# Performance work log

Measured on AMD Instinct MI355X. Metric: run time of the kernel, lower is better.

Reference implementation:

```python
import jax, jax.numpy as jnp
import numpy as np

# Model dims (match init_kwargs / input_specs)
L, D, H, F = 4, 1024, 16, 4096   # layers, d_model, heads, ffn hidden
B, S = 4, 1024                    # batch, seq_len
HD = D // H                       # head dim = 64
K = 8                             # context-mask band width (k=8, 2//k == 0)
LN_EPS = 1e-5


def setup_inputs():
    key = jax.random.key(0)
    ks = jax.random.split(key, 16)
    s = 0.02  # init scale for weights
    return {
        "src":   jax.random.normal(ks[0], (B, S, D), jnp.float32),
        # stacked per-layer params (leading dim L)
        "Wqkv":  jax.random.normal(ks[1], (L, 3 * D, D), jnp.float32) * s,
        "bqkv":  jnp.zeros((L, 3 * D), jnp.float32),
        "Wo":    jax.random.normal(ks[2], (L, D, D), jnp.float32) * s,
        "bo":    jnp.zeros((L, D), jnp.float32),
        "W1":    jax.random.normal(ks[3], (L, F, D), jnp.float32) * s,
        "b1":    jnp.zeros((L, F), jnp.float32),
        "W2":    jax.random.normal(ks[4], (L, D, F), jnp.float32) * s,
        "b2":    jnp.zeros((L, D), jnp.float32),
        "ln1_w": jnp.ones((L, D), jnp.float32),
        "ln1_b": jnp.zeros((L, D), jnp.float32),
        "ln2_w": jnp.ones((L, D), jnp.float32),
        "ln2_b": jnp.zeros((L, D), jnp.float32),
    }


def _layer_norm(x, g, b):
    m = jnp.mean(x, axis=-1, keepdims=True)
    v = jnp.mean(jnp.square(x - m), axis=-1, keepdims=True)
    return (x - m) * jax.lax.rsqrt(v + LN_EPS) * g + b


def _context_mask(sz):
    # row i allows keys j with i <= j < i + K (clamped into range); 0 allowed, -inf masked
    i = jnp.arange(sz)[:, None]
    j = jnp.arange(sz)[None, :]
    return jnp.where((j >= i) & (j < i + K), 0.0, -jnp.inf).astype(jnp.float32)


def reference(src, Wqkv, bqkv, Wo, bo, W1, b1, W2, b2, ln1_w, ln1_b, ln2_w, ln2_b):
    mask = _context_mask(S)  # [S, S] additive mask
    scale = 1.0 / jnp.sqrt(jnp.float32(HD))
    x = src  # [B, S, D] (batch-first; equivalent to torch's permute round-trip)
    for l in range(L):
        # --- self-attention (post-norm, dropout=0) ---
        qkv = jnp.einsum('bsd,ed->bse', x, Wqkv[l]) + bqkv[l]  # [B,S,3D]
        q, k, v = jnp.split(qkv, 3, axis=-1)
        q = q.reshape(B, S, H, HD).transpose(0, 2, 1, 3)  # [B,H,S,HD]
        k = k.reshape(B, S, H, HD).transpose(0, 2, 1, 3)
        v = v.reshape(B, S, H, HD).transpose(0, 2, 1, 3)
        scores = jnp.einsum('bhqd,bhkd->bhqk', q, k) * scale + mask
        attn = jax.nn.softmax(scores, axis=-1)
        o = jnp.einsum('bhqk,bhkd->bhqd', attn, v)
        o = o.transpose(0, 2, 1, 3).reshape(B, S, D)
        o = jnp.einsum('bsd,ed->bse', o, Wo[l]) + bo[l]
        x = _layer_norm(x + o, ln1_w[l], ln1_b[l])
        # --- feed-forward, exact (erf) gelu ---
        h = jax.nn.gelu(jnp.einsum('bsd,fd->bsf', x, W1[l]) + b1[l], approximate=False)
        h = jnp.einsum('bsf,df->bsd', h, W2[l]) + b2[l]
        x = _layer_norm(x + h, ln2_w[l], ln2_b[l])
    return x
```

## Files before the change

kernel.cpp:

```cpp
#include <hip/hip_runtime.h>

#define LNUM 4
#define DMODEL 1024
#define NHEAD 16
#define FDIM 4096
#define BATCH 4
#define SEQ 1024
#define HDIM 64
#define KBAND 8
#define MROWS (BATCH * SEQ)

typedef __attribute__((ext_vector_type(8))) __bf16 bf16x8;
typedef __attribute__((ext_vector_type(4))) float f32x4;

__device__ __forceinline__ unsigned short f2bf(float f) {
  unsigned int u = __builtin_bit_cast(unsigned int, f);
  u = u + 0x7fffu + ((u >> 16) & 1u);
  return (unsigned short)(u >> 16);
}
__device__ __forceinline__ float bf2f(unsigned short h) {
  unsigned int u = ((unsigned int)h) << 16;
  return __builtin_bit_cast(float, u);
}

#define GLOAD16(gp, lp)                                                        \
  __builtin_amdgcn_global_load_lds(                                            \
      (const __attribute__((address_space(1))) void*)(gp),                     \
      (__attribute__((address_space(3))) void*)(lp), 16, 0, 0)

__global__ __launch_bounds__(256) void cvt_bf16(const float* __restrict__ in,
                                                unsigned short* __restrict__ out,
                                                long n) {
  long i = ((long)blockIdx.x * 256 + threadIdx.x) * 4;
  if (i + 3 < n) {
    float4 v = *reinterpret_cast<const float4*>(in + i);
    ushort4 o;
    o.x = f2bf(v.x);
    o.y = f2bf(v.y);
    o.z = f2bf(v.z);
    o.w = f2bf(v.w);
    *reinterpret_cast<ushort4*>(out + i) = o;
  }
}

#define BAR_MID()                                                              \
  __builtin_amdgcn_s_barrier();                                                \
  asm volatile("s_waitcnt lgkmcnt(0)" ::: "memory");                           \
  __builtin_amdgcn_sched_barrier(0)

#define BAR_END()                                                              \
  __builtin_amdgcn_s_barrier();                                                \
  __builtin_amdgcn_sched_barrier(0)

template <int EPI>
__global__ __launch_bounds__(512, 2) void gemm256(const unsigned short* __restrict__ A,
                                                  const unsigned short* __restrict__ W,
                                                  const float* __restrict__ bias,
                                                  unsigned short* __restrict__ Cout,
                                                  int Ndim, int Kdim, int Ks) {
  __shared__ unsigned short As[2][16384];
  __shared__ unsigned short Bs[2][16384];
  const int tid = threadIdx.x;
  const int wave = tid >> 6;
  const int lane = tid & 63;
  const int wm = wave >> 2;
  const int wn = wave & 3;

  const int gx = gridDim.x, gy = gridDim.y;
  const int nwg = gx * gy;
  const int lin = blockIdx.x + blockIdx.y * gx;
  const int q8 = nwg >> 3, r8 = nwg & 7;
  const int xcd = lin & 7, cidx = lin >> 3;
  const int cbase = (xcd < r8) ? xcd * (q8 + 1) : r8 * (q8 + 1) + (xcd - r8) * q8;
  const int swz = cbase + cidx;
  const int bm0 = (swz % gy) * 256;
  const int bn0 = (swz / gy) * 256;
  const int kz0 = blockIdx.z * Ks;

  const int r0 = tid >> 3;
  const int c0 = (((tid & 7) ^ ((tid >> 3) & 7)) << 3);
  const size_t rowstep = (size_t)64 * Kdim;

#define STAGEH(MAT, rowg, buf, LDSARR, h, kt)                                  \
  do {                                                                         \
    const unsigned short* g = MAT + (size_t)((rowg) + (h) * 128 + r0) * Kdim + \
                              kz0 + (kt) * 64 + c0;                            \
    char* lb = (char*)&LDSARR[buf][0] + (h) * 16384 + wave * 1024;             \
    GLOAD16(g, lb);                                                            \
    GLOAD16(g + rowstep, lb + 8192);                                           \
  } while (0)

  const int fr = lane & 15;
  const int kc = (lane >> 4) * 8;
  const int fsw = (fr & 7) << 3;
  bf16x8 A0[2][4], A1[2][4], Bv[2][2];
  f32x4 acc[2][2][4][2] = {};

#define RD_A(SET, buf, rh)                                                     \
  _Pragma("unroll") for (int ks = 0; ks < 2; ++ks)                             \
      _Pragma("unroll") for (int fi = 0; fi < 4; ++fi)                         \
      SET[ks][fi] = *reinterpret_cast<const bf16x8*>(                          \
          &As[buf][(wm * 128 + (rh) * 64 + fi * 16 + fr) * 64 +                \
                   ((ks * 32 + kc) ^ fsw)]);

#define RD_B(buf, ch)                                                          \
  _Pragma("unroll") for (int ks = 0; ks < 2; ++ks)                             \
      _Pragma("unroll") for (int fj = 0; fj < 2; ++fj)                         \
      Bv[ks][fj] = *reinterpret_cast<const bf16x8*>(                           \
          &Bs[buf][(wn * 64 + (ch) * 32 + fj * 16 + fr) * 64 +                 \
                   ((ks * 32 + kc) ^ fsw)]);

#define MFMA_Q(rh, ch, ASET)                                                   \
  __builtin_amdgcn_s_setprio(1);                                               \
  _Pragma("unroll") for (int ks = 0; ks < 2; ++ks)                             \
      _Pragma("unroll") for (int fi = 0; fi < 4; ++fi)                         \
      _Pragma("unroll") for (int fj = 0; fj < 2; ++fj)                         \
      acc[rh][ch][fi][fj] = __builtin_amdgcn_mfma_f32_16x16x32_bf16(           \
          ASET[ks][fi], Bv[ks][fj], acc[rh][ch][fi][fj], 0, 0, 0);             \
  __builtin_amdgcn_s_setprio(0)

  const int nt = Ks >> 6;
  STAGEH(A, bm0, 0, As, 0, 0);
  STAGEH(A, bm0, 0, As, 1, 0);
  STAGEH(W, bn0, 0, Bs, 0, 0);
  STAGEH(W, bn0, 0, Bs, 1, 0);
  STAGEH(A, bm0, 1, As, 0, 1);
  STAGEH(A, bm0, 1, As, 1, 1);
  STAGEH(W, bn0, 1, Bs, 0, 1);
  asm volatile("s_waitcnt vmcnt(6)" ::: "memory");
  BAR_END();

  const int npair = nt >> 1;
  for (int i = 0; i < npair; ++i) {
    const int t1 = 2 * i + 1, t2 = 2 * i + 2, t3 = 2 * i + 3;
    const bool pf = (t2 < nt);
    RD_A(A0, 0, 0);
    RD_B(0, 0);
    STAGEH(W, bn0, 1, Bs, 1, t1);
    BAR_MID();
    MFMA_Q(0, 0, A0);
    BAR_END();

    RD_A(A1, 0, 1);
    BAR_MID();
    MFMA_Q(1, 0, A1);
    BAR_END();

    RD_B(0, 1);
    if (pf) STAGEH(A, bm0, 0, As, 0, t2);
    BAR_MID();
    MFMA_Q(1, 1, A1);
    BAR_END();

    if (pf) {
      STAGEH(A, bm0, 0, As, 1, t2);
      STAGEH(W, bn0, 0, Bs, 0, t2);
    }
    BAR_MID();
    MFMA_Q(0, 1, A0);
    if (pf)
      asm volatile("s_waitcnt vmcnt(6)" ::: "memory");
    else
      asm volatile("s_waitcnt vmcnt(0)" ::: "memory");
    BAR_END();

    RD_A(A0, 1, 0);
    RD_B(1, 0);
    if (pf) STAGEH(W, bn0, 0, Bs, 1, t2);
    BAR_MID();
    MFMA_Q(0, 0, A0);
    BAR_END();

    RD_A(A1, 1, 1);
    BAR_MID();
    MFMA_Q(1, 0, A1);
    BAR_END();

    RD_B(1, 1);
    if (pf) STAGEH(A, bm0, 1, As, 0, t3);
    BAR_MID();
    MFMA_Q(1, 1, A1);
    BAR_END();

    if (pf) {
      STAGEH(A, bm0, 1, As, 1, t3);
      STAGEH(W, bn0, 1, Bs, 0, t3);
    }
    BAR_MID();
    MFMA_Q(0, 1, A0);
    if (pf) asm volatile("s_waitcnt vmcnt(6)" ::: "memory");
    BAR_END();
  }

#undef STAGEH
#undef RD_A
#undef RD_B
#undef MFMA_Q

  const int rr = (lane >> 4) * 4;
  const int cc = lane & 15;
  const bool addb = (EPI != 2) || (blockIdx.z == 0);
  unsigned short* outZ =
      Cout + (EPI == 2 ? (size_t)blockIdx.z * ((size_t)gy * 256) * Ndim : 0);
#pragma unroll
  for (int rh = 0; rh < 2; ++rh)
#pragma unroll
    for (int ch = 0; ch < 2; ++ch)
#pragma unroll
      for (int fj = 0; fj < 2; ++fj) {
        const int n = bn0 + wn * 64 + ch * 32 + fj * 16 + cc;
        const float bv = addb ? bias[n] : 0.0f;
#pragma unroll
        for (int fi = 0; fi < 4; ++fi)
#pragma unroll
          for (int r = 0; r < 4; ++r) {
            const int m = bm0 + wm * 128 + rh * 64 + fi * 16 + rr + r;
            float v = acc[rh][ch][fi][fj][r] + bv;
            if (EPI == 1) v = 0.5f * v * (1.0f + erff(v * 0.70710678118654752f));
            outZ[(size_t)m * Ndim + n] = f2bf(v);
          }
      }
}

__global__ __launch_bounds__(256) void attn_band(const unsigned short* __restrict__ qkv,
                                                 unsigned short* __restrict__ outp) {
  const int gw = blockIdx.x * 4 + (threadIdx.x >> 6);
  const int lane = threadIdx.x & 63;
  const int q = gw & (SEQ - 1);
  const int bh = gw >> 10;
  const int h = bh & (NHEAD - 1);
  const int b = bh >> 4;
  const size_t row0 = (size_t)(b * SEQ + q);
  const size_t stride = 3 * DMODEL;
  const float qv = bf2f(qkv[row0 * stride + h * HDIM + lane]);

  float sc[KBAND];
  float mx = -1e30f;
#pragma unroll
  for (int jj = 0; jj < KBAND; ++jj) {
    const int j = q + jj;
    const int jc = (j < SEQ) ? j : (SEQ - 1);
    float kv = bf2f(qkv[(size_t)(b * SEQ + jc) * stride + DMODEL + h * HDIM + lane]);
    float p = qv * kv;
#pragma unroll
    for (int m = 32; m; m >>= 1) p += __shfl_xor(p, m);
    p *= 0.125f;
    p = (j < SEQ) ? p : -1e30f;
    sc[jj] = p;
    mx = fmaxf(mx, p);
  }
  float denom = 0.f;
  float ov = 0.f;
#pragma unroll
  for (int jj = 0; jj < KBAND; ++jj) {
    const int j = q + jj;
    const int jc = (j < SEQ) ? j : (SEQ - 1);
    float p = __expf(sc[jj] - mx);
    p = (j < SEQ) ? p : 0.f;
    denom += p;
    ov += p * bf2f(qkv[(size_t)(b * SEQ + jc) * stride + 2 * DMODEL + h * HDIM + lane]);
  }
  ov /= denom;
  outp[row0 * DMODEL + h * HDIM + lane] = f2bf(ov);
}

__global__ __launch_bounds__(256) void add_ln4(const float* __restrict__ resid,
                                               const unsigned short* __restrict__ part,
                                               const float* __restrict__ gw,
                                               const float* __restrict__ gb,
                                               float* __restrict__ xf,
                                               unsigned short* __restrict__ xb) {
  const int row = blockIdx.x;
  const int tid = threadIdx.x;
  const size_t slab = (size_t)MROWS * DMODEL;
  const float* rp = resid + (size_t)row * DMODEL;
  const unsigned short* pp = part + (size_t)row * DMODEL;
  float v[4];
  float s = 0.f, s2 = 0.f;
#pragma unroll
  for (int i = 0; i < 4; ++i) {
    const int idx = tid + i * 256;
    float a = rp[idx];
#pragma unroll
    for (int z = 0; z < 4; ++z) a += bf2f(pp[z * slab + idx]);
    v[i] = a;
    s += a;
    s2 += a * a;
  }
#pragma unroll
  for (int m = 32; m; m >>= 1) {
    s += __shfl_xor(s, m);
    s2 += __shfl_xor(s2, m);
  }
  __shared__ float wsm[8];
  const int wave = tid >> 6, lane = tid & 63;
  if (lane == 0) {
    wsm[wave] = s;
    wsm[4 + wave] = s2;
  }
  __syncthreads();
  s = wsm[0] + wsm[1] + wsm[2] + wsm[3];
  s2 = wsm[4] + wsm[5] + wsm[6] + wsm[7];
  const float mean = s * (1.f / DMODEL);
  const float var = s2 * (1.f / DMODEL) - mean * mean;
  const float rstd = rsqrtf(var + 1e-5f);
#pragma unroll
  for (int i = 0; i < 4; ++i) {
    const int idx = tid + i * 256;
    const float y = (v[i] - mean) * rstd * gw[idx] + gb[idx];
    xf[(size_t)row * DMODEL + idx] = y;
    xb[(size_t)row * DMODEL + idx] = f2bf(y);
  }
}

extern "C" void kernel_launch(void* const* d_in, const int* in_sizes, int n_in,
                              void* d_out, int out_size, void* d_ws, size_t ws_size,
                              hipStream_t stream) {
  const float* src  = (const float*)d_in[0];
  const float* Wqkv = (const float*)d_in[1];
  const float* bqkv = (const float*)d_in[2];
  const float* Wo   = (const float*)d_in[3];
  const float* bo   = (const float*)d_in[4];
  const float* W1   = (const float*)d_in[5];
  const float* b1   = (const float*)d_in[6];
  const float* W2   = (const float*)d_in[7];
  const float* b2   = (const float*)d_in[8];
  const float* ln1w = (const float*)d_in[9];
  const float* ln1b = (const float*)d_in[10];
  const float* ln2w = (const float*)d_in[11];
  const float* ln2b = (const float*)d_in[12];
  float* out = (float*)d_out;

  char* p = (char*)d_ws;
  unsigned short* wqkv_b = (unsigned short*)p; p += (size_t)LNUM * 3072 * 1024 * 2;
  unsigned short* wo_b   = (unsigned short*)p; p += (size_t)LNUM * 1024 * 1024 * 2;
  unsigned short* w1_b   = (unsigned short*)p; p += (size_t)LNUM * 4096 * 1024 * 2;
  unsigned short* w2_b   = (unsigned short*)p; p += (size_t)LNUM * 1024 * 4096 * 2;
  float*          xf     = (float*)p;          p += (size_t)MROWS * DMODEL * 4;
  unsigned short* xb     = (unsigned short*)p; p += (size_t)MROWS * DMODEL * 2;
  char* R = p;
  unsigned short* qkvb = (unsigned short*)R;
  unsigned short* aob  = (unsigned short*)(R + (size_t)MROWS * 3 * DMODEL * 2);
  unsigned short* hb   = (unsigned short*)R;
  unsigned short* part = (unsigned short*)(R + (size_t)MROWS * 4096 * 2);
  p = R + (size_t)MROWS * 4096 * 2 + (size_t)4 * MROWS * DMODEL * 2;
  if (ws_size < (size_t)(p - (char*)d_ws)) return;

  cvt_bf16<<<(long)LNUM * 3072 * 1024 / 1024, 256, 0, stream>>>(Wqkv, wqkv_b, (long)LNUM * 3072 * 1024);
  cvt_bf16<<<(long)LNUM * 1024 * 1024 / 1024, 256, 0, stream>>>(Wo, wo_b, (long)LNUM * 1024 * 1024);
  cvt_bf16<<<(long)LNUM * 4096 * 1024 / 1024, 256, 0, stream>>>(W1, w1_b, (long)LNUM * 4096 * 1024);
  cvt_bf16<<<(long)LNUM * 1024 * 4096 / 1024, 256, 0, stream>>>(W2, w2_b, (long)LNUM * 1024 * 4096);
  cvt_bf16<<<(long)MROWS * DMODEL / 1024, 256, 0, stream>>>(src, xb, (long)MROWS * DMODEL);

  for (int l = 0; l < LNUM; ++l) {
    gemm256<0><<<dim3(3072 / 256, MROWS / 256, 1), 512, 0, stream>>>(
        xb, wqkv_b + (size_t)l * 3072 * 1024, bqkv + l * 3072, qkvb, 3072, 1024, 1024);
    attn_band<<<(BATCH * NHEAD * SEQ) / 4, 256, 0, stream>>>(qkvb, aob);
    gemm256<2><<<dim3(1024 / 256, MROWS / 256, 4), 512, 0, stream>>>(
        aob, wo_b + (size_t)l * 1024 * 1024, bo + l * 1024, part, 1024, 1024, 256);
    add_ln4<<<MROWS, 256, 0, stream>>>(l == 0 ? src : xf, part,
                                       ln1w + l * DMODEL, ln1b + l * DMODEL, xf, xb);
    gemm256<1><<<dim3(FDIM / 256, MROWS / 256, 1), 512, 0, stream>>>(
        xb, w1_b + (size_t)l * 4096 * 1024, b1 + l * FDIM, hb, FDIM, 1024, 1024);
    gemm256<2><<<dim3(1024 / 256, MROWS / 256, 4), 512, 0, stream>>>(
        hb, w2_b + (size_t)l * 1024 * 4096, b2 + l * 1024, part, 1024, 4096, 1024);
    float* dst = (l == LNUM - 1) ? out : xf;
    add_ln4<<<MROWS, 256, 0, stream>>>(xf, part,
                                       ln2w + l * DMODEL, ln2b + l * DMODEL, dst, xb);
  }
}
```

Before: 984.8 us.

## Stage GEMM epilogue through LDS for vectorized 16-byte bf16 stores

The GEMM epilogue now writes each 64x16 accumulator sub-tile into a per-wave LDS scratch region that reuses the A tile buffer. Each lane then reads back one row, applies bias and the optional GELU, and writes 16 contiguous bf16 values with two 16-byte stores, replacing scattered 2-byte stores. The barrier macros also drop their sched_barrier fences, which gives the compiler more freedom to schedule across the main loop. The LDS reuse has no block barrier after the loop, so other waves may still be reading the A buffer, and the row-major reads (lane*16 float stride) can cause LDS bank conflicts.

Result: slower. 1.101 ms (+11.8%).

```diff
diff --git a/kernel.cpp b/kernel.cpp
--- a/kernel.cpp
+++ b/kernel.cpp
@@ -12,6 +12,7 @@
 
 typedef __attribute__((ext_vector_type(8))) __bf16 bf16x8;
 typedef __attribute__((ext_vector_type(4))) float f32x4;
+typedef __attribute__((ext_vector_type(8))) unsigned short u16x8;
 
 __device__ __forceinline__ unsigned short f2bf(float f) {
   unsigned int u = __builtin_bit_cast(unsigned int, f);
@@ -45,12 +46,9 @@
 
 #define BAR_MID()                                                              \
   __builtin_amdgcn_s_barrier();                                                \
-  asm volatile("s_waitcnt lgkmcnt(0)" ::: "memory");                           \
-  __builtin_amdgcn_sched_barrier(0)
-
-#define BAR_END()                                                              \
-  __builtin_amdgcn_s_barrier();                                                \
-  __builtin_amdgcn_sched_barrier(0)
+  asm volatile("s_waitcnt lgkmcnt(0)" ::: "memory")
+
+#define BAR_END() __builtin_amdgcn_s_barrier()
 
 template <int EPI>
 __global__ __launch_bounds__(512, 2) void gemm256(const unsigned short* __restrict__ A,
@@ -202,24 +200,35 @@
   const bool addb = (EPI != 2) || (blockIdx.z == 0);
   unsigned short* outZ =
       Cout + (EPI == 2 ? (size_t)blockIdx.z * ((size_t)gy * 256) * Ndim : 0);
-#pragma unroll
-  for (int rh = 0; rh < 2; ++rh)
-#pragma unroll
-    for (int ch = 0; ch < 2; ++ch)
-#pragma unroll
-      for (int fj = 0; fj < 2; ++fj) {
-        const int n = bn0 + wn * 64 + ch * 32 + fj * 16 + cc;
-        const float bv = addb ? bias[n] : 0.0f;
-#pragma unroll
-        for (int fi = 0; fi < 4; ++fi)
-#pragma unroll
-          for (int r = 0; r < 4; ++r) {
-            const int m = bm0 + wm * 128 + rh * 64 + fi * 16 + rr + r;
-            float v = acc[rh][ch][fi][fj][r] + bv;
-            if (EPI == 1) v = 0.5f * v * (1.0f + erff(v * 0.70710678118654752f));
-            outZ[(size_t)m * Ndim + n] = f2bf(v);
-          }
-      }
+  float* lt = (float*)&As[0][0] + wave * 1024;
+#pragma unroll
+  for (int s = 0; s < 8; ++s) {
+    const int rh = s >> 2, ch = (s >> 1) & 1, fj = s & 1;
+#pragma unroll
+    for (int fi = 0; fi < 4; ++fi)
+#pragma unroll
+      for (int r = 0; r < 4; ++r)
+        lt[(fi * 16 + rr + r) * 16 + cc] = acc[rh][ch][fi][fj][r];
+    asm volatile("s_waitcnt lgkmcnt(0)" ::: "memory");
+    const int n0 = bn0 + wn * 64 + ch * 32 + fj * 16;
+    const int m = bm0 + wm * 128 + rh * 64 + lane;
+    u16x8 o0, o1;
+#pragma unroll
+    for (int j = 0; j < 8; ++j) {
+      float v = lt[lane * 16 + j] + (addb ? bias[n0 + j] : 0.0f);
+      if (EPI == 1) v = 0.5f * v * (1.0f + erff(v * 0.70710678118654752f));
+      o0[j] = f2bf(v);
+    }
+#pragma unroll
+    for (int j = 0; j < 8; ++j) {
+      float v = lt[lane * 16 + 8 + j] + (addb ? bias[n0 + 8 + j] : 0.0f);
+      if (EPI == 1) v = 0.5f * v * (1.0f + erff(v * 0.70710678118654752f));
+      o1[j] = f2bf(v);
+    }
+    unsigned short* dst = outZ + (size_t)m * Ndim + n0;
+    *reinterpret_cast<u16x8*>(dst) = o0;
+    *reinterpret_cast<u16x8*>(dst + 8) = o1;
+  }
 }
 
 __global__ __launch_bounds__(256) void attn_band(const unsigned short* __restrict__ qkv,
```

## Replace phased GEMM main loop with simple double-buffered tile loop

Applied to the files above, without the earlier changes.

The hand-scheduled eight-phase main loop in the 256x256 bf16 GEMM is removed. It interleaved partial LDS reads, async global-to-LDS staging and MFMA quadrants with fine-grained barriers, priority hints and vmcnt waits. In its place is a plain double-buffered loop: stage the next full K tile, read all A/B fragments of the current tile, run all MFMAs, then __syncthreads. This cuts code complexity and barrier count per tile. The risk is losing the overlap between LDS reads, global loads and MFMA issue, and raising register pressure from holding all fragments at once.

New measurement: 952.0 us. 3.3% less time.

```diff
diff --git a/kernel.cpp b/kernel.cpp
--- a/kernel.cpp
+++ b/kernel.cpp
@@ -42,15 +42,6 @@
     *reinterpret_cast<ushort4*>(out + i) = o;
   }
 }
-
-#define BAR_MID()                                                              \
-  __builtin_amdgcn_s_barrier();                                                \
-  asm volatile("s_waitcnt lgkmcnt(0)" ::: "memory");                           \
-  __builtin_amdgcn_sched_barrier(0)
-
-#define BAR_END()                                                              \
-  __builtin_amdgcn_s_barrier();                                                \
-  __builtin_amdgcn_sched_barrier(0)
 
 template <int EPI>
 __global__ __launch_bounds__(512, 2) void gemm256(const unsigned short* __restrict__ A,
@@ -90,112 +81,66 @@
     GLOAD16(g + rowstep, lb + 8192);                                           \
   } while (0)
 
+#define STAGE_TILE(buf, kt)                                                    \
+  do {                                                                         \
+    STAGEH(A, bm0, buf, As, 0, kt);                                            \
+    STAGEH(A, bm0, buf, As, 1, kt);                                            \
+    STAGEH(W, bn0, buf, Bs, 0, kt);                                            \
+    STAGEH(W, bn0, buf, Bs, 1, kt);                                            \
+  } while (0)
+
   const int fr = lane & 15;
   const int kc = (lane >> 4) * 8;
   const int fsw = (fr & 7) << 3;
-  bf16x8 A0[2][4], A1[2][4], Bv[2][2];
   f32x4 acc[2][2][4][2] = {};
 
-#define RD_A(SET, buf, rh)                                                     \
-  _Pragma("unroll") for (int ks = 0; ks < 2; ++ks)                             \
-      _Pragma("unroll") for (int fi = 0; fi < 4; ++fi)                         \
-      SET[ks][fi] = *reinterpret_cast<const bf16x8*>(                          \
-          &As[buf][(wm * 128 + (rh) * 64 + fi * 16 + fr) * 64 +                \
-                   ((ks * 32 + kc) ^ fsw)]);
-
-#define RD_B(buf, ch)                                                          \
-  _Pragma("unroll") for (int ks = 0; ks < 2; ++ks)                             \
-      _Pragma("unroll") for (int fj = 0; fj < 2; ++fj)                         \
-      Bv[ks][fj] = *reinterpret_cast<const bf16x8*>(                           \
-          &Bs[buf][(wn * 64 + (ch) * 32 + fj * 16 + fr) * 64 +                 \
-                   ((ks * 32 + kc) ^ fsw)]);
-
-#define MFMA_Q(rh, ch, ASET)                                                   \
-  __builtin_amdgcn_s_setprio(1);                                               \
-  _Pragma("unroll") for (int ks = 0; ks < 2; ++ks)                             \
-      _Pragma("unroll") for (int fi = 0; fi < 4; ++fi)                         \
-      _Pragma("unroll") for (int fj = 0; fj < 2; ++fj)                         \
-      acc[rh][ch][fi][fj] = __builtin_amdgcn_mfma_f32_16x16x32_bf16(           \
-          ASET[ks][fi], Bv[ks][fj], acc[rh][ch][fi][fj], 0, 0, 0);             \
-  __builtin_amdgcn_s_setprio(0)
-
   const int nt = Ks >> 6;
-  STAGEH(A, bm0, 0, As, 0, 0);
-  STAGEH(A, bm0, 0, As, 1, 0);
-  STAGEH(W, bn0, 0, Bs, 0, 0);
-  STAGEH(W, bn0, 0, Bs, 1, 0);
-  STAGEH(A, bm0, 1, As, 0, 1);
-  STAGEH(A, bm0, 1, As, 1, 1);
-  STAGEH(W, bn0, 1, Bs, 0, 1);
-  asm volatile("s_waitcnt vmcnt(6)" ::: "memory");
-  BAR_END();
-
-  const int npair = nt >> 1;
-  for (int i = 0; i < npair; ++i) {
-    const int t1 = 2 * i + 1, t2 = 2 * i + 2, t3 = 2 * i + 3;
-    const bool pf = (t2 < nt);
-    RD_A(A0, 0, 0);
-    RD_B(0, 0);
-    STAGEH(W, bn0, 1, Bs, 1, t1);
-    BAR_MID();
-    MFMA_Q(0, 0, A0);
-    BAR_END();
-
-    RD_A(A1, 0, 1);
-    BAR_MID();
-    MFMA_Q(1, 0, A1);
-    BAR_END();
-
-    RD_B(0, 1);
-    if (pf) STAGEH(A, bm0, 0, As, 0, t2);
-    BAR_MID();
-    MFMA_Q(1, 1, A1);
-    BAR_END();
-
-    if (pf) {
-      STAGEH(A, bm0, 0, As, 1, t2);
-      STAGEH(W, bn0, 0, Bs, 0, t2);
-    }
-    BAR_MID();
-    MFMA_Q(0, 1, A0);
-    if (pf)
-      asm volatile("s_waitcnt vmcnt(6)" ::: "memory");
-    else
-      asm volatile("s_waitcnt vmcnt(0)" ::: "memory");
-    BAR_END();
-
-    RD_A(A0, 1, 0);
-    RD_B(1, 0);
-    if (pf) STAGEH(W, bn0, 0, Bs, 1, t2);
-    BAR_MID();
-    MFMA_Q(0, 0, A0);
-    BAR_END();
-
-    RD_A(A1, 1, 1);
-    BAR_MID();
-    MFMA_Q(1, 0, A1);
-    BAR_END();
-
-    RD_B(1, 1);
-    if (pf) STAGEH(A, bm0, 1, As, 0, t3);
-    BAR_MID();
-    MFMA_Q(1, 1, A1);
-    BAR_END();
-
-    if (pf) {
-      STAGEH(A, bm0, 1, As, 1, t3);
-      STAGEH(W, bn0, 1, Bs, 0, t3);
-    }
-    BAR_MID();
-    MFMA_Q(0, 1, A0);
-    if (pf) asm volatile("s_waitcnt vmcnt(6)" ::: "memory");
-    BAR_END();
+  STAGE_TILE(0, 0);
+  asm volatile("s_waitcnt vmcnt(0)" ::: "memory");
+  __builtin_amdgcn_s_barrier();
+
+  for (int t = 0; t < nt; ++t) {
+    const int cur = t & 1;
+    if (t + 1 < nt) STAGE_TILE(cur ^ 1, t + 1);
+
+    bf16x8 Af[2][2][4], Bf[2][2][2];
+#pragma unroll
+    for (int rh = 0; rh < 2; ++rh)
+#pragma unroll
+      for (int ks = 0; ks < 2; ++ks)
+#pragma unroll
+        for (int fi = 0; fi < 4; ++fi)
+          Af[rh][ks][fi] = *reinterpret_cast<const bf16x8*>(
+              &As[cur][(wm * 128 + rh * 64 + fi * 16 + fr) * 64 +
+                       ((ks * 32 + kc) ^ fsw)]);
+#pragma unroll
+    for (int ch = 0; ch < 2; ++ch)
+#pragma unroll
+      for (int ks = 0; ks < 2; ++ks)
+#pragma unroll
+        for (int fj = 0; fj < 2; ++fj)
+          Bf[ch][ks][fj] = *reinterpret_cast<const bf16x8*>(
+              &Bs[cur][(wn * 64 + ch * 32 + fj * 16 + fr) * 64 +
+                       ((ks * 32 + kc) ^ fsw)]);
+
+#pragma unroll
+    for (int rh = 0; rh < 2; ++rh)
+#pragma unroll
+      for (int ch = 0; ch < 2; ++ch)
+#pragma unroll
+        for (int ks = 0; ks < 2; ++ks)
+#pragma unroll
+          for (int fi = 0; fi < 4; ++fi)
+#pragma unroll
+            for (int fj = 0; fj < 2; ++fj)
+              acc[rh][ch][fi][fj] = __builtin_amdgcn_mfma_f32_16x16x32_bf16(
+                  Af[rh][ks][fi], Bf[ch][ks][fj], acc[rh][ch][fi][fj], 0, 0, 0);
+
+    __syncthreads();
   }
 
 #undef STAGEH
-#undef RD_A
-#undef RD_B
-#undef MFMA_Q
+#undef STAGE_TILE
 
   const int rr = (lane >> 4) * 4;
   const int cc = lane & 15;
```
